# Performance work log

Hardware: AMD Instinct MI355X
Metric: run time of the kernel (lower is better)

## Reference

```python
import jax, jax.numpy as jnp
import numpy as np

N_SENT, B, S, D = 256, 512, 128, 1024
L, LATENT = 10331, 101  # int(sqrt(10331)) == 101


def setup_inputs() -> dict:
    key = jax.random.key(0)
    ks = jax.random.split(key, 16)
    inv = 1.0 / np.sqrt(D)
    return {
        'elmo_outputs': jax.random.normal(ks[0], (N_SENT, S, D), jnp.float32),
        'men_mask': jax.random.randint(ks[1], (B, S), 0, 2).astype(jnp.float32),
        'ctx_mask': jax.random.randint(ks[2], (B, S), 0, 2).astype(jnp.float32),
        'dist': jax.random.uniform(ks[3], (B, S), jnp.float32),
        'gathers': jax.random.randint(ks[4], (B,), 0, N_SENT),
        # nn.Linear weights, stored [out, in] as in torch
        'W_men_m': jax.random.normal(ks[5], (D, D), jnp.float32) * inv,
        'W_men_o': jax.random.normal(ks[6], (1, D), jnp.float32) * inv,
        'W_ctx_c': jax.random.normal(ks[7], (D, D), jnp.float32) * inv,
        'W_ctx_m': jax.random.normal(ks[8], (D, D), jnp.float32) * inv,
        'w_ctx_d': jax.random.normal(ks[9], (D,), jnp.float32),  # Linear(1, D) weight [D,1] squeezed
        'W_ctx_o': jax.random.normal(ks[10], (1, D), jnp.float32) * inv,
        'W_out': jax.random.normal(ks[11], (L, 2 * D), jnp.float32) * (1.0 / np.sqrt(2 * D)),
        'W_f2l': jax.random.normal(ks[12], (LATENT, 2 * D), jnp.float32) * (1.0 / np.sqrt(2 * D)),
        'W_l2l': jax.random.normal(ks[13], (L, LATENT), jnp.float32) * (1.0 / np.sqrt(LATENT)),
        'latent_scalar': jnp.array(0.1, jnp.float32),
    }


def reference(elmo_outputs, men_mask, ctx_mask, dist, gathers,
              W_men_m, W_men_o, W_ctx_c, W_ctx_m, w_ctx_d, W_ctx_o,
              W_out, W_f2l, W_l2l, latent_scalar):
    NEG = -10000.0
    # gather: sentence reps -> mention rows, [B, S, D]
    x = elmo_outputs[gathers]
    # mention additive attention
    men_h = jnp.tanh(jnp.einsum('bsd,ed->bse', x, W_men_m))
    men_score = jnp.einsum('bse,oe->bso', men_h, W_men_o)  # [B,S,1]
    men_score = men_score + (1.0 - men_mask[:, :, None]) * NEG
    men_attn = jax.nn.softmax(men_score, axis=1)
    men_repr = jnp.sum(x * men_attn, axis=1)  # [B, D]
    # context additive attention (dropout layers are identity in eval)
    ctx_h = jnp.tanh(
        jnp.einsum('bsd,ed->bse', x, W_ctx_c)
        + jnp.einsum('bd,ed->be', men_repr, W_ctx_m)[:, None, :]
        + dist[:, :, None] * w_ctx_d
    )
    ctx_score = jnp.einsum('bse,oe->bso', ctx_h, W_ctx_o)
    ctx_score = ctx_score + (1.0 - ctx_mask[:, :, None]) * NEG
    ctx_attn = jax.nn.softmax(ctx_score, axis=1)
    ctx_repr = jnp.sum(x * ctx_attn, axis=1)  # [B, D]
    final_repr = jnp.concatenate([men_repr, ctx_repr], axis=1)  # [B, 2D]
    outputs = final_repr @ W_out.T  # [B, L]
    latent_label = final_repr @ W_f2l.T  # [B, latent]
    outputs_latent = latent_label @ W_l2l.T  # [B, L]
    outputs = outputs + latent_scalar * outputs_latent
    return outputs, outputs_latent
```

## Files before the change

### kernel.cpp

```cpp
#include <hip/hip_runtime.h>
#include <hip/hip_bf16.h>

typedef __bf16 bf16x8 __attribute__((ext_vector_type(8)));
typedef float f32x4 __attribute__((ext_vector_type(4)));
typedef unsigned short u16x8 __attribute__((ext_vector_type(8)));

#define DEV __device__ __forceinline__

static constexpr int N_SENTC = 256, BB = 512, SS = 128, DD = 1024;
static constexpr int LL = 10331, LATENT = 101;
static constexpr int LPAD = 10368;
static constexpr int LATPAD = 128;

DEV float bf2f(unsigned short u) {
  unsigned v = (unsigned)u << 16;
  return __builtin_bit_cast(float, v);
}
DEV unsigned short f2bf(float f) {
  unsigned u = __builtin_bit_cast(unsigned, f);
  unsigned lsb = (u >> 16) & 1u;
  u += 0x7fffu + lsb;
  return (unsigned short)(u >> 16);
}

DEV void stage8(unsigned short* dst, const float* src) {
  float4 a = *(const float4*)src;
  float4 b = *(const float4*)(src + 4);
  unsigned short t[8];
  t[0] = f2bf(a.x); t[1] = f2bf(a.y); t[2] = f2bf(a.z); t[3] = f2bf(a.w);
  t[4] = f2bf(b.x); t[5] = f2bf(b.y); t[6] = f2bf(b.z); t[7] = f2bf(b.w);
  *(uint4*)dst = *(uint4*)t;
}

DEV void gl_lds16(const unsigned short* g, unsigned short* l) {
  __builtin_amdgcn_global_load_lds(
      (const __attribute__((address_space(1))) unsigned int*)g,
      (__attribute__((address_space(3))) unsigned int*)l, 16, 0, 0);
}

__global__ __launch_bounds__(256) void k_cvt(
    const float* __restrict__ src, unsigned short* __restrict__ dst, int n4) {
  for (int i = blockIdx.x * 256 + threadIdx.x; i < n4; i += gridDim.x * 256) {
    float4 v = ((const float4*)src)[i];
    unsigned short t[4] = {f2bf(v.x), f2bf(v.y), f2bf(v.z), f2bf(v.w)};
    ((uint2*)dst)[i] = *(const uint2*)t;
  }
}

__global__ __launch_bounds__(256) void k_cvt_pad(
    const float* __restrict__ src, unsigned short* __restrict__ dst,
    int srcR, int srcC, int dstC, int total) {
  for (int i = blockIdx.x * 256 + threadIdx.x; i < total; i += gridDim.x * 256) {
    int r = i / dstC, c = i - r * dstC;
    dst[i] = (r < srcR && c < srcC) ? f2bf(src[(size_t)r * srcC + c]) : (unsigned short)0;
  }
}

__global__ __launch_bounds__(256) void k_mc_gemm(
    const unsigned short* __restrict__ Xb, const unsigned short* __restrict__ Wmb,
    const unsigned short* __restrict__ Wcb, const float* __restrict__ wo,
    float* __restrict__ score, unsigned short* __restrict__ Hc) {
  __shared__ __align__(16) unsigned short As[2 * 128 * 32];
  __shared__ __align__(16) unsigned short Bs[2 * 128 * 32];
  const int colTile = blockIdx.x;
  const int rowBase = blockIdx.y * 128;
  const bool isMen = colTile < 8;
  const unsigned short* __restrict__ Bsrc = isMen ? Wmb : Wcb;
  const int bcolBase = (isMen ? colTile : colTile - 8) * 128;
  const int tid = threadIdx.x, wave = tid >> 6, lane = tid & 63;
  const int lm = lane & 15, lq = lane >> 4;
  const int wr = (wave & 1) * 64, wc = (wave >> 1) * 64;
  const int srow = wave * 32 + (lane >> 2);
  const int scol = (lane & 3) * 8;
  const unsigned short* aPtr = Xb + (size_t)(rowBase + srow) * 1024 + scol;
  const unsigned short* bPtr = Bsrc + (size_t)(bcolBase + srow) * 1024 + scol;
  f32x4 acc[4][4] = {};
  for (int k0 = 0; k0 < 1024; k0 += 64) {
    __syncthreads();
#pragma unroll
    for (int h = 0; h < 2; ++h) {
      gl_lds16(aPtr + k0 + h * 32, As + h * 4096 + wave * 1024);
      gl_lds16(aPtr + k0 + h * 32 + 16 * 1024, As + h * 4096 + wave * 1024 + 512);
      gl_lds16(bPtr + k0 + h * 32, Bs + h * 4096 + wave * 1024);
      gl_lds16(bPtr + k0 + h * 32 + 16 * 1024, Bs + h * 4096 + wave * 1024 + 512);
    }
    __syncthreads();
#pragma unroll
    for (int h = 0; h < 2; ++h) {
      bf16x8 af[4], bfr[4];
#pragma unroll
      for (int m = 0; m < 4; ++m)
        af[m] = *(const bf16x8*)&As[h * 4096 + (wr + m * 16 + lm) * 32 + lq * 8];
#pragma unroll
      for (int n = 0; n < 4; ++n)
        bfr[n] = *(const bf16x8*)&Bs[h * 4096 + (wc + n * 16 + lm) * 32 + lq * 8];
#pragma unroll
      for (int m = 0; m < 4; ++m)
#pragma unroll
        for (int n = 0; n < 4; ++n)
          acc[m][n] = __builtin_amdgcn_mfma_f32_16x16x32_bf16(af[m], bfr[n], acc[m][n], 0, 0, 0);
    }
  }
  if (isMen) {
    float wov[4];
#pragma unroll
    for (int n = 0; n < 4; ++n) wov[n] = wo[bcolBase + wc + n * 16 + lm];
    float rsum[4][4];
#pragma unroll
    for (int m = 0; m < 4; ++m)
#pragma unroll
      for (int r = 0; r < 4; ++r) {
        float s = 0.f;
#pragma unroll
        for (int n = 0; n < 4; ++n) s += tanhf(acc[m][n][r]) * wov[n];
        rsum[m][r] = s;
      }
#pragma unroll
    for (int msk = 1; msk <= 8; msk <<= 1)
#pragma unroll
      for (int m = 0; m < 4; ++m)
#pragma unroll
        for (int r = 0; r < 4; ++r) rsum[m][r] += __shfl_xor(rsum[m][r], msk, 64);
    if (lm == 0) {
#pragma unroll
      for (int m = 0; m < 4; ++m)
#pragma unroll
        for (int r = 0; r < 4; ++r)
          atomicAdd(&score[rowBase + wr + m * 16 + lq * 4 + r], rsum[m][r]);
    }
  } else {
#pragma unroll
    for (int m = 0; m < 4; ++m)
#pragma unroll
      for (int n = 0; n < 4; ++n) {
        int col = bcolBase + wc + n * 16 + lm;
#pragma unroll
        for (int r = 0; r < 4; ++r) {
          int row = rowBase + wr + m * 16 + lq * 4 + r;
          Hc[(size_t)row * 1024 + col] = f2bf(acc[m][n][r]);
        }
      }
  }
}

__global__ __launch_bounds__(256) void k_ctx_score(
    const unsigned short* __restrict__ Hc, const int* __restrict__ gathers,
    const float* __restrict__ cb, const float* __restrict__ wd,
    const float* __restrict__ wo, const float* __restrict__ dist,
    float* __restrict__ score) {
  const int b = blockIdx.x, tid = threadIdx.x, wave = tid >> 6, lane = tid & 63;
  const int n = gathers[b];
  __shared__ float cbl[1024], wdl[1024], wol[1024];
  for (int i = tid; i < 1024; i += 256) {
    cbl[i] = cb[b * 1024 + i];
    wdl[i] = wd[i];
    wol[i] = wo[i];
  }
  __syncthreads();
  for (int s = wave; s < 128; s += 4) {
    float d = dist[b * 128 + s];
    const unsigned short* hrow = &Hc[(size_t)(n * 128 + s) * 1024 + lane * 16];
    unsigned short hs[16];
    *(uint4*)hs = *(const uint4*)hrow;
    *(uint4*)(hs + 8) = *(const uint4*)(hrow + 8);
    float p = 0.f;
#pragma unroll
    for (int j = 0; j < 16; ++j) {
      int e = lane * 16 + j;
      p += tanhf(bf2f(hs[j]) + cbl[e] + d * wdl[e]) * wol[e];
    }
#pragma unroll
    for (int msk = 1; msk <= 32; msk <<= 1) p += __shfl_xor(p, msk, 64);
    if (lane == 0) score[b * 128 + s] = p;
  }
}

__global__ __launch_bounds__(256) void k_softb(
    const float* __restrict__ score_src, const float* __restrict__ mask,
    const unsigned short* __restrict__ Xb, const int* __restrict__ gathers,
    unsigned short* __restrict__ finalrb, int isCtx) {
  const int b = blockIdx.x, tid = threadIdx.x;
  const int n = gathers[b];
  __shared__ float attn[128];
  __shared__ float red[128 * 8];
  __shared__ float smax, ssum;
  if (tid < 128) {
    int srow = isCtx ? b : n;
    attn[tid] = score_src[srow * 128 + tid] + (1.0f - mask[b * 128 + tid]) * (-10000.0f);
  }
  __syncthreads();
  if (tid == 0) {
    float m = attn[0];
    for (int i = 1; i < 128; ++i) m = fmaxf(m, attn[i]);
    smax = m;
  }
  __syncthreads();
  if (tid < 128) attn[tid] = expf(attn[tid] - smax);
  __syncthreads();
  if (tid == 0) {
    float s = 0.f;
    for (int i = 0; i < 128; ++i) s += attn[i];
    ssum = 1.0f / s;
  }
  __syncthreads();
  if (tid < 128) attn[tid] *= ssum;
  __syncthreads();
  const unsigned short* xb = Xb + (size_t)n * 128 * 1024;
  const int c = tid & 127, h = tid >> 7;
  float acc[8] = {};
  for (int s = h; s < 128; s += 2) {
    float w = attn[s];
    u16x8 v = *(const u16x8*)&xb[(size_t)s * 1024 + c * 8];
#pragma unroll
    for (int j = 0; j < 8; ++j) acc[j] += w * bf2f(v[j]);
  }
  if (h == 1) {
#pragma unroll
    for (int j = 0; j < 8; ++j) red[c * 8 + j] = acc[j];
  }
  __syncthreads();
  if (h == 0) {
    unsigned short o[8];
#pragma unroll
    for (int j = 0; j < 8; ++j) o[j] = f2bf(acc[j] + red[c * 8 + j]);
    *(uint4*)&finalrb[(size_t)b * 2048 + (isCtx ? 1024 : 0) + c * 8] = *(uint4*)o;
  }
}

__global__ __launch_bounds__(256) void k_cb_gemm_b(
    const unsigned short* __restrict__ finalrb, const unsigned short* __restrict__ Wcmb,
    float* __restrict__ cb) {
  __shared__ __align__(16) unsigned short As[64 * 32];
  __shared__ __align__(16) unsigned short Bs[64 * 32];
  const int bid = blockIdx.x;
  const int rowBase = (bid >> 4) * 64, colBase = (bid & 15) * 64;
  const int tid = threadIdx.x, wave = tid >> 6, lane = tid & 63;
  const int lm = lane & 15, lq = lane >> 4;
  const int sr = tid >> 2, sc = (tid & 3) * 8;
  f32x4 acc[4] = {};
  for (int k0 = 0; k0 < 1024; k0 += 32) {
    __syncthreads();
    *(uint4*)&As[sr * 32 + sc] = *(const uint4*)&finalrb[(size_t)(rowBase + sr) * 2048 + k0 + sc];
    *(uint4*)&Bs[sr * 32 + sc] = *(const uint4*)&Wcmb[(size_t)(colBase + sr) * 1024 + k0 + sc];
    __syncthreads();
    bf16x8 af = *(const bf16x8*)&As[(wave * 16 + lm) * 32 + lq * 8];
#pragma unroll
    for (int j = 0; j < 4; ++j) {
      bf16x8 bfr = *(const bf16x8*)&Bs[(j * 16 + lm) * 32 + lq * 8];
      acc[j] = __builtin_amdgcn_mfma_f32_16x16x32_bf16(af, bfr, acc[j], 0, 0, 0);
    }
  }
#pragma unroll
  for (int j = 0; j < 4; ++j) {
    int col = colBase + j * 16 + lm;
#pragma unroll
    for (int r = 0; r < 4; ++r) {
      int row = rowBase + wave * 16 + lq * 4 + r;
      cb[row * 1024 + col] = acc[j][r];
    }
  }
}

__global__ __launch_bounds__(256) void k_lat_gemm_b(
    const unsigned short* __restrict__ finalrb, const unsigned short* __restrict__ Wf2lb,
    unsigned short* __restrict__ latb) {
  __shared__ __align__(16) unsigned short As[64 * 32];
  __shared__ __align__(16) unsigned short Bs[64 * 32];
  const int rowBase = blockIdx.y * 64, colBase = blockIdx.x * 64;
  const int tid = threadIdx.x, wave = tid >> 6, lane = tid & 63;
  const int lm = lane & 15, lq = lane >> 4;
  const int sr = tid >> 2, sc = (tid & 3) * 8;
  f32x4 acc[4] = {};
  for (int k0 = 0; k0 < 2048; k0 += 32) {
    __syncthreads();
    *(uint4*)&As[sr * 32 + sc] = *(const uint4*)&finalrb[(size_t)(rowBase + sr) * 2048 + k0 + sc];
    *(uint4*)&Bs[sr * 32 + sc] = *(const uint4*)&Wf2lb[(size_t)(colBase + sr) * 2048 + k0 + sc];
    __syncthreads();
    bf16x8 af = *(const bf16x8*)&As[(wave * 16 + lm) * 32 + lq * 8];
#pragma unroll
    for (int j = 0; j < 4; ++j) {
      bf16x8 bfr = *(const bf16x8*)&Bs[(j * 16 + lm) * 32 + lq * 8];
      acc[j] = __builtin_amdgcn_mfma_f32_16x16x32_bf16(af, bfr, acc[j], 0, 0, 0);
    }
  }
#pragma unroll
  for (int j = 0; j < 4; ++j) {
    int col = colBase + j * 16 + lm;
#pragma unroll
    for (int r = 0; r < 4; ++r) {
      int row = rowBase + wave * 16 + lq * 4 + r;
      latb[row * LATPAD + col] = f2bf(acc[j][r]);
    }
  }
}

__global__ __launch_bounds__(256) void k_out_gemm_b(
    const unsigned short* __restrict__ finalrb, const unsigned short* __restrict__ Woutb,
    const unsigned short* __restrict__ latb, const unsigned short* __restrict__ Wl2lb,
    const float* __restrict__ lscale, float* __restrict__ out,
    float* __restrict__ outLat) {
  __shared__ __align__(16) unsigned short As[2 * 128 * 32];
  __shared__ __align__(16) unsigned short Bs[2 * 128 * 32];
  const int colBase = blockIdx.x * 128;
  const int rowBase = blockIdx.y * 128;
  const int tid = threadIdx.x, wave = tid >> 6, lane = tid & 63;
  const int lm = lane & 15, lq = lane >> 4;
  const int wr = (wave & 1) * 64, wc = (wave >> 1) * 64;
  const int srow = wave * 32 + (lane >> 2);
  const int scol = (lane & 3) * 8;
  const float scal = lscale[0];
  const unsigned short* aPtr = finalrb + (size_t)(rowBase + srow) * 2048 + scol;
  const unsigned short* bPtr = Woutb + (size_t)(colBase + srow) * 2048 + scol;
  f32x4 acc[4][4] = {};
  for (int k0 = 0; k0 < 2048; k0 += 64) {
    __syncthreads();
#pragma unroll
    for (int h = 0; h < 2; ++h) {
      gl_lds16(aPtr + k0 + h * 32, As + h * 4096 + wave * 1024);
      gl_lds16(aPtr + k0 + h * 32 + 16 * 2048, As + h * 4096 + wave * 1024 + 512);
      gl_lds16(bPtr + k0 + h * 32, Bs + h * 4096 + wave * 1024);
      gl_lds16(bPtr + k0 + h * 32 + 16 * 2048, Bs + h * 4096 + wave * 1024 + 512);
    }
    __syncthreads();
#pragma unroll
    for (int h = 0; h < 2; ++h) {
      bf16x8 af[4], bfr[4];
#pragma unroll
      for (int m = 0; m < 4; ++m)
        af[m] = *(const bf16x8*)&As[h * 4096 + (wr + m * 16 + lm) * 32 + lq * 8];
#pragma unroll
      for (int n = 0; n < 4; ++n)
        bfr[n] = *(const bf16x8*)&Bs[h * 4096 + (wc + n * 16 + lm) * 32 + lq * 8];
#pragma unroll
      for (int m = 0; m < 4; ++m)
#pragma unroll
        for (int n = 0; n < 4; ++n)
          acc[m][n] = __builtin_amdgcn_mfma_f32_16x16x32_bf16(af[m], bfr[n], acc[m][n], 0, 0, 0);
    }
  }
  const unsigned short* aPtr2 = latb + (size_t)(rowBase + srow) * LATPAD + scol;
  const unsigned short* bPtr2 = Wl2lb + (size_t)(colBase + srow) * LATPAD + scol;
  f32x4 acc2[4][4] = {};
  for (int k0 = 0; k0 < 128; k0 += 64) {
    __syncthreads();
#pragma unroll
    for (int h = 0; h < 2; ++h) {
      gl_lds16(aPtr2 + k0 + h * 32, As + h * 4096 + wave * 1024);
      gl_lds16(aPtr2 + k0 + h * 32 + 16 * LATPAD, As + h * 4096 + wave * 1024 + 512);
      gl_lds16(bPtr2 + k0 + h * 32, Bs + h * 4096 + wave * 1024);
      gl_lds16(bPtr2 + k0 + h * 32 + 16 * LATPAD, Bs + h * 4096 + wave * 1024 + 512);
    }
    __syncthreads();
#pragma unroll
    for (int h = 0; h < 2; ++h) {
      bf16x8 af[4], bfr[4];
#pragma unroll
      for (int m = 0; m < 4; ++m)
        af[m] = *(const bf16x8*)&As[h * 4096 + (wr + m * 16 + lm) * 32 + lq * 8];
#pragma unroll
      for (int n = 0; n < 4; ++n)
        bfr[n] = *(const bf16x8*)&Bs[h * 4096 + (wc + n * 16 + lm) * 32 + lq * 8];
#pragma unroll
      for (int m = 0; m < 4; ++m)
#pragma unroll
        for (int n = 0; n < 4; ++n)
          acc2[m][n] = __builtin_amdgcn_mfma_f32_16x16x32_bf16(af[m], bfr[n], acc2[m][n], 0, 0, 0);
    }
  }
#pragma unroll
  for (int m = 0; m < 4; ++m)
#pragma unroll
    for (int n = 0; n < 4; ++n) {
      int col = colBase + wc + n * 16 + lm;
      if (col < LL) {
#pragma unroll
        for (int r = 0; r < 4; ++r) {
          int row = rowBase + wr + m * 16 + lq * 4 + r;
          float lv = acc2[m][n][r];
          out[(size_t)row * LL + col] = acc[m][n][r] + scal * lv;
          outLat[(size_t)row * LL + col] = lv;
        }
      }
    }
}

__global__ __launch_bounds__(256) void k_men_gemm(
    const float* __restrict__ X, const float* __restrict__ Wm,
    const float* __restrict__ wo, float* __restrict__ score) {
  __shared__ __align__(16) unsigned short As[64 * 32];
  __shared__ __align__(16) unsigned short Bs[64 * 32];
  const int bid = blockIdx.x;
  const int rowBase = (bid >> 4) * 64, colBase = (bid & 15) * 64;
  const int tid = threadIdx.x, wave = tid >> 6, lane = tid & 63;
  const int lm = lane & 15, lq = lane >> 4;
  const int sr = tid >> 2, sc = (tid & 3) * 8;
  f32x4 acc[4] = {};
  for (int k0 = 0; k0 < 1024; k0 += 32) {
    __syncthreads();
    stage8(&As[sr * 32 + sc], &X[(size_t)(rowBase + sr) * 1024 + k0 + sc]);
    stage8(&Bs[sr * 32 + sc], &Wm[(size_t)(colBase + sr) * 1024 + k0 + sc]);
    __syncthreads();
    bf16x8 af = *(const bf16x8*)&As[(wave * 16 + lm) * 32 + lq * 8];
#pragma unroll
    for (int j = 0; j < 4; ++j) {
      bf16x8 bfr = *(const bf16x8*)&Bs[(j * 16 + lm) * 32 + lq * 8];
      acc[j] = __builtin_amdgcn_mfma_f32_16x16x32_bf16(af, bfr, acc[j], 0, 0, 0);
    }
  }
  float rsum[4] = {0.f, 0.f, 0.f, 0.f};
#pragma unroll
  for (int j = 0; j < 4; ++j) {
    float w = wo[colBase + j * 16 + lm];
#pragma unroll
    for (int r = 0; r < 4; ++r) rsum[r] += tanhf(acc[j][r]) * w;
  }
#pragma unroll
  for (int m = 1; m <= 8; m <<= 1)
#pragma unroll
    for (int r = 0; r < 4; ++r) rsum[r] += __shfl_xor(rsum[r], m, 64);
  if (lm == 0) {
    int row0 = rowBase + wave * 16 + lq * 4;
#pragma unroll
    for (int r = 0; r < 4; ++r) atomicAdd(&score[row0 + r], rsum[r]);
  }
}

__global__ __launch_bounds__(256) void k_ctx_gemm(
    const float* __restrict__ X, const int* __restrict__ gathers,
    const float* __restrict__ Wc, const float* __restrict__ wd,
    const float* __restrict__ wo, const float* __restrict__ dist,
    const float* __restrict__ cb, float* __restrict__ score) {
  __shared__ __align__(16) unsigned short As[64 * 32];
  __shared__ __align__(16) unsigned short Bs[64 * 32];
  const int bid = blockIdx.x;
  const int rowBase = (bid >> 4) * 64, colBase = (bid & 15) * 64;
  const int tid = threadIdx.x, wave = tid >> 6, lane = tid & 63;
  const int lm = lane & 15, lq = lane >> 4;
  const int sr = tid >> 2, sc = (tid & 3) * 8;
  const int row_g = rowBase + sr;
  const int srcRow = (gathers[row_g >> 7] << 7) + (row_g & 127);
  f32x4 acc[4] = {};
  for (int k0 = 0; k0 < 1024; k0 += 32) {
    __syncthreads();
    stage8(&As[sr * 32 + sc], &X[(size_t)srcRow * 1024 + k0 + sc]);
    stage8(&Bs[sr * 32 + sc], &Wc[(size_t)(colBase + sr) * 1024 + k0 + sc]);
    __syncthreads();
    bf16x8 af = *(const bf16x8*)&As[(wave * 16 + lm) * 32 + lq * 8];
#pragma unroll
    for (int j = 0; j < 4; ++j) {
      bf16x8 bfr = *(const bf16x8*)&Bs[(j * 16 + lm) * 32 + lq * 8];
      acc[j] = __builtin_amdgcn_mfma_f32_16x16x32_bf16(af, bfr, acc[j], 0, 0, 0);
    }
  }
  float rsum[4] = {0.f, 0.f, 0.f, 0.f};
#pragma unroll
  for (int j = 0; j < 4; ++j) {
    int col = colBase + j * 16 + lm;
    float w = wo[col];
    float wdv = wd[col];
#pragma unroll
    for (int r = 0; r < 4; ++r) {
      int rg = rowBase + wave * 16 + lq * 4 + r;
      int b = rg >> 7, s = rg & 127;
      float v = acc[j][r] + cb[b * 1024 + col] + dist[b * 128 + s] * wdv;
      rsum[r] += tanhf(v) * w;
    }
  }
#pragma unroll
  for (int m = 1; m <= 8; m <<= 1)
#pragma unroll
    for (int r = 0; r < 4; ++r) rsum[r] += __shfl_xor(rsum[r], m, 64);
  if (lm == 0) {
    int row0 = rowBase + wave * 16 + lq * 4;
#pragma unroll
    for (int r = 0; r < 4; ++r) atomicAdd(&score[row0 + r], rsum[r]);
  }
}

__global__ __launch_bounds__(256) void k_soft(
    const float* __restrict__ score_src, const float* __restrict__ mask,
    const float* __restrict__ X, const int* __restrict__ gathers,
    float* __restrict__ finalr, int isCtx) {
  const int b = blockIdx.x, tid = threadIdx.x;
  const int n = gathers[b];
  __shared__ float attn[128];
  __shared__ float smax, ssum;
  if (tid < 128) {
    int srow = isCtx ? b : n;
    attn[tid] = score_src[srow * 128 + tid] + (1.0f - mask[b * 128 + tid]) * (-10000.0f);
  }
  __syncthreads();
  if (tid == 0) {
    float m = attn[0];
    for (int i = 1; i < 128; ++i) m = fmaxf(m, attn[i]);
    smax = m;
  }
  __syncthreads();
  if (tid < 128) attn[tid] = expf(attn[tid] - smax);
  __syncthreads();
  if (tid == 0) {
    float s = 0.f;
    for (int i = 0; i < 128; ++i) s += attn[i];
    ssum = 1.0f / s;
  }
  __syncthreads();
  if (tid < 128) attn[tid] *= ssum;
  __syncthreads();
  const float* xb = &X[(size_t)(n << 7) * 1024];
  const int off = isCtx ? 1024 : 0;
  for (int d = tid; d < 1024; d += 256) {
    float a = 0.f;
#pragma unroll 8
    for (int s = 0; s < 128; ++s) a += attn[s] * xb[s * 1024 + d];
    finalr[b * 2048 + off + d] = a;
  }
}

__global__ __launch_bounds__(256) void k_cb_gemm(
    const float* __restrict__ finalr, const float* __restrict__ Wcm,
    float* __restrict__ cb) {
  __shared__ __align__(16) unsigned short As[64 * 32];
  __shared__ __align__(16) unsigned short Bs[64 * 32];
  const int bid = blockIdx.x;
  const int rowBase = (bid >> 4) * 64, colBase = (bid & 15) * 64;
  const int tid = threadIdx.x, wave = tid >> 6, lane = tid & 63;
  const int lm = lane & 15, lq = lane >> 4;
  const int sr = tid >> 2, sc = (tid & 3) * 8;
  f32x4 acc[4] = {};
  for (int k0 = 0; k0 < 1024; k0 += 32) {
    __syncthreads();
    stage8(&As[sr * 32 + sc], &finalr[(size_t)(rowBase + sr) * 2048 + k0 + sc]);
    stage8(&Bs[sr * 32 + sc], &Wcm[(size_t)(colBase + sr) * 1024 + k0 + sc]);
    __syncthreads();
    bf16x8 af = *(const bf16x8*)&As[(wave * 16 + lm) * 32 + lq * 8];
#pragma unroll
    for (int j = 0; j < 4; ++j) {
      bf16x8 bfr = *(const bf16x8*)&Bs[(j * 16 + lm) * 32 + lq * 8];
      acc[j] = __builtin_amdgcn_mfma_f32_16x16x32_bf16(af, bfr, acc[j], 0, 0, 0);
    }
  }
#pragma unroll
  for (int j = 0; j < 4; ++j) {
    int col = colBase + j * 16 + lm;
#pragma unroll
    for (int r = 0; r < 4; ++r) {
      int row = rowBase + wave * 16 + lq * 4 + r;
      cb[row * 1024 + col] = acc[j][r];
    }
  }
}

__global__ __launch_bounds__(256) void k_lat_gemm(
    const float* __restrict__ finalr, const float* __restrict__ Wf2l,
    float* __restrict__ lat) {
  __shared__ __align__(16) unsigned short As[64 * 32];
  __shared__ __align__(16) unsigned short Bs[64 * 32];
  const int rowBase = blockIdx.y * 64, colBase = blockIdx.x * 64;
  const int tid = threadIdx.x, wave = tid >> 6, lane = tid & 63;
  const int lm = lane & 15, lq = lane >> 4;
  const int sr = tid >> 2, sc = (tid & 3) * 8;
  f32x4 acc[4] = {};
  for (int k0 = 0; k0 < 2048; k0 += 32) {
    __syncthreads();
    stage8(&As[sr * 32 + sc], &finalr[(size_t)(rowBase + sr) * 2048 + k0 + sc]);
    int l = colBase + sr;
    if (l < LATENT) {
      stage8(&Bs[sr * 32 + sc], &Wf2l[(size_t)l * 2048 + k0 + sc]);
    } else {
      uint4 z = {0, 0, 0, 0};
      *(uint4*)&Bs[sr * 32 + sc] = z;
    }
    __syncthreads();
    bf16x8 af = *(const bf16x8*)&As[(wave * 16 + lm) * 32 + lq * 8];
#pragma unroll
    for (int j = 0; j < 4; ++j) {
      bf16x8 bfr = *(const bf16x8*)&Bs[(j * 16 + lm) * 32 + lq * 8];
      acc[j] = __builtin_amdgcn_mfma_f32_16x16x32_bf16(af, bfr, acc[j], 0, 0, 0);
    }
  }
#pragma unroll
  for (int j = 0; j < 4; ++j) {
    int col = colBase + j * 16 + lm;
    if (col < LATENT) {
#pragma unroll
      for (int r = 0; r < 4; ++r) {
        int row = rowBase + wave * 16 + lq * 4 + r;
        lat[row * LATENT + col] = acc[j][r];
      }
    }
  }
}

__global__ __launch_bounds__(256) void k_out_gemm(
    const float* __restrict__ finalr, const float* __restrict__ Wout,
    const float* __restrict__ lat, const float* __restrict__ Wl2l,
    const float* __restrict__ lscale, float* __restrict__ out,
    float* __restrict__ outLat) {
  __shared__ __align__(16) unsigned short As[64 * 32];
  __shared__ __align__(16) unsigned short Bs[64 * 32];
  const int rowBase = blockIdx.y * 64, colBase = blockIdx.x * 64;
  const int tid = threadIdx.x, wave = tid >> 6, lane = tid & 63;
  const int lm = lane & 15, lq = lane >> 4;
  const int sr = tid >> 2, sc = (tid & 3) * 8;
  const float scal = lscale[0];
  const int lrow = colBase + sr;
  const bool lvalid = (lrow < LL);
  f32x4 acc[4] = {};
  for (int k0 = 0; k0 < 2048; k0 += 32) {
    __syncthreads();
    stage8(&As[sr * 32 + sc], &finalr[(size_t)(rowBase + sr) * 2048 + k0 + sc]);
    if (lvalid) {
      stage8(&Bs[sr * 32 + sc], &Wout[(size_t)lrow * 2048 + k0 + sc]);
    } else {
      uint4 z = {0, 0, 0, 0};
      *(uint4*)&Bs[sr * 32 + sc] = z;
    }
    __syncthreads();
    bf16x8 af = *(const bf16x8*)&As[(wave * 16 + lm) * 32 + lq * 8];
#pragma unroll
    for (int j = 0; j < 4; ++j) {
      bf16x8 bfr = *(const bf16x8*)&Bs[(j * 16 + lm) * 32 + lq * 8];
      acc[j] = __builtin_amdgcn_mfma_f32_16x16x32_bf16(af, bfr, acc[j], 0, 0, 0);
    }
  }
  f32x4 acc2[4] = {};
  for (int k2 = 0; k2 < 128; k2 += 32) {
    __syncthreads();
    const int brow = rowBase + sr;
#pragma unroll
    for (int jj = 0; jj < 8; ++jj) {
      int idx = k2 + sc + jj;
      As[sr * 32 + sc + jj] = (idx < LATENT) ? f2bf(lat[brow * LATENT + idx]) : (unsigned short)0;
      Bs[sr * 32 + sc + jj] = (lvalid && idx < LATENT) ? f2bf(Wl2l[lrow * LATENT + idx]) : (unsigned short)0;
    }
    __syncthreads();
    bf16x8 af = *(const bf16x8*)&As[(wave * 16 + lm) * 32 + lq * 8];
#pragma unroll
    for (int j = 0; j < 4; ++j) {
      bf16x8 bfr = *(const bf16x8*)&Bs[(j * 16 + lm) * 32 + lq * 8];
      acc2[j] = __builtin_amdgcn_mfma_f32_16x16x32_bf16(af, bfr, acc2[j], 0, 0, 0);
    }
  }
#pragma unroll
  for (int j = 0; j < 4; ++j) {
    int col = colBase + j * 16 + lm;
    if (col < LL) {
#pragma unroll
      for (int r = 0; r < 4; ++r) {
        int row = rowBase + wave * 16 + lq * 4 + r;
        float lv = acc2[j][r];
        out[(size_t)row * LL + col] = acc[j][r] + scal * lv;
        outLat[(size_t)row * LL + col] = lv;
      }
    }
  }
}

extern "C" void kernel_launch(void* const* d_in, const int* in_sizes, int n_in,
                              void* d_out, int out_size, void* d_ws, size_t ws_size,
                              hipStream_t stream) {
  const float* X = (const float*)d_in[0];
  const float* men_mask = (const float*)d_in[1];
  const float* ctx_mask = (const float*)d_in[2];
  const float* dist = (const float*)d_in[3];
  const int* gathers = (const int*)d_in[4];
  const float* W_men_m = (const float*)d_in[5];
  const float* W_men_o = (const float*)d_in[6];
  const float* W_ctx_c = (const float*)d_in[7];
  const float* W_ctx_m = (const float*)d_in[8];
  const float* w_ctx_d = (const float*)d_in[9];
  const float* W_ctx_o = (const float*)d_in[10];
  const float* W_out = (const float*)d_in[11];
  const float* W_f2l = (const float*)d_in[12];
  const float* W_l2l = (const float*)d_in[13];
  const float* lscale = (const float*)d_in[14];
  float* out = (float*)d_out;
  float* outLat = out + (size_t)BB * LL;

  size_t off = 0;
  auto carve = [&](size_t bytes) {
    void* p = (char*)d_ws + off;
    off = (off + bytes + 255) & ~(size_t)255;
    return p;
  };
  float* sent_score = (float*)carve(32768 * 4);
  float* ctx_score = (float*)carve(65536 * 4);
  float* finalr = (float*)carve((size_t)512 * 2048 * 4);
  float* cb = (float*)carve((size_t)512 * 1024 * 4);
  float* lat = (float*)carve((size_t)512 * LATENT * 4);
  unsigned short* Xb = (unsigned short*)carve((size_t)32768 * 1024 * 2);
  unsigned short* Wmb = (unsigned short*)carve((size_t)1024 * 1024 * 2);
  unsigned short* Wcb = (unsigned short*)carve((size_t)1024 * 1024 * 2);
  unsigned short* Wcmb = (unsigned short*)carve((size_t)1024 * 1024 * 2);
  unsigned short* Hc = (unsigned short*)carve((size_t)32768 * 1024 * 2);
  unsigned short* Wf2lb = (unsigned short*)carve((size_t)LATPAD * 2048 * 2);
  unsigned short* Wl2lb = (unsigned short*)carve((size_t)LPAD * LATPAD * 2);
  unsigned short* finalrb = (unsigned short*)carve((size_t)512 * 2048 * 2);
  unsigned short* latb = (unsigned short*)carve((size_t)512 * LATPAD * 2);
  const bool fits = off <= ws_size;
  unsigned short* Woutb = Xb;

  if (fits) {
    hipMemsetAsync(sent_score, 0, 32768 * sizeof(float), stream);
    k_cvt<<<8192, 256, 0, stream>>>(X, Xb, 32768 * 1024 / 4);
    k_cvt<<<1024, 256, 0, stream>>>(W_men_m, Wmb, 1024 * 1024 / 4);
    k_cvt<<<1024, 256, 0, stream>>>(W_ctx_c, Wcb, 1024 * 1024 / 4);
    k_cvt<<<1024, 256, 0, stream>>>(W_ctx_m, Wcmb, 1024 * 1024 / 4);
    k_cvt_pad<<<512, 256, 0, stream>>>(W_f2l, Wf2lb, LATENT, 2048, 2048, LATPAD * 2048);
    k_cvt_pad<<<1024, 256, 0, stream>>>(W_l2l, Wl2lb, LL, LATENT, LATPAD, LPAD * LATPAD);
    k_mc_gemm<<<dim3(16, 256), 256, 0, stream>>>(Xb, Wmb, Wcb, W_men_o, sent_score, Hc);
    k_softb<<<512, 256, 0, stream>>>(sent_score, men_mask, Xb, gathers, finalrb, 0);
    k_cb_gemm_b<<<128, 256, 0, stream>>>(finalrb, Wcmb, cb);
    k_ctx_score<<<512, 256, 0, stream>>>(Hc, gathers, cb, w_ctx_d, W_ctx_o, dist, ctx_score);
    k_softb<<<512, 256, 0, stream>>>(ctx_score, ctx_mask, Xb, gathers, finalrb, 1);
    k_lat_gemm_b<<<dim3(2, 8), 256, 0, stream>>>(finalrb, Wf2lb, latb);
    k_cvt_pad<<<8192, 256, 0, stream>>>(W_out, Woutb, LL, 2048, 2048, LPAD * 2048);
    k_out_gemm_b<<<dim3(81, 4), 256, 0, stream>>>(finalrb, Woutb, latb, Wl2lb,
                                                  lscale, out, outLat);
  } else {
    hipMemsetAsync(d_ws, 0, (32768 + 65536) * sizeof(float), stream);
    k_men_gemm<<<8192, 256, 0, stream>>>(X, W_men_m, W_men_o, sent_score);
    k_soft<<<512, 256, 0, stream>>>(sent_score, men_mask, X, gathers, finalr, 0);
    k_cb_gemm<<<128, 256, 0, stream>>>(finalr, W_ctx_m, cb);
    k_ctx_gemm<<<16384, 256, 0, stream>>>(X, gathers, W_ctx_c, w_ctx_d, W_ctx_o, dist, cb, ctx_score);
    k_soft<<<512, 256, 0, stream>>>(ctx_score, ctx_mask, X, gathers, finalr, 1);
    k_lat_gemm<<<dim3(2, 8), 256, 0, stream>>>(finalr, W_f2l, lat);
    k_out_gemm<<<dim3(162, 8), 256, 0, stream>>>(finalr, W_out, lat, W_l2l, lscale, out, outLat);
  }
}
```

Before: 740.9 us.

## Rewrite mention/context GEMM as 256x256 8-wave pipelined kernel with swizzled LDS

Replaces the 128x128 tile, 4-wave GEMM with a 256x256 tile, 8-wave kernel. It double-buffers LDS, interleaves global-to-LDS loads with MFMA phases, and uses s_setprio and manual vmcnt waits. LDS columns are XOR-swizzled to avoid bank conflicts, and block IDs are remapped so blocks sharing weight tiles run close together for L2 reuse. The goal is better MFMA utilisation and less memory stall on the largest GEMM, at the cost of more registers and fragile hand-written barrier and wait counts.

```diff
diff --git a/kernel.cpp b/kernel.cpp
--- a/kernel.cpp
+++ b/kernel.cpp
@@ -56,58 +56,131 @@
   }
 }
 
-__global__ __launch_bounds__(256) void k_mc_gemm(
+__global__ __launch_bounds__(512) void k_mc_gemm8(
     const unsigned short* __restrict__ Xb, const unsigned short* __restrict__ Wmb,
     const unsigned short* __restrict__ Wcb, const float* __restrict__ wo,
     float* __restrict__ score, unsigned short* __restrict__ Hc) {
-  __shared__ __align__(16) unsigned short As[2 * 128 * 32];
-  __shared__ __align__(16) unsigned short Bs[2 * 128 * 32];
-  const int colTile = blockIdx.x;
-  const int rowBase = blockIdx.y * 128;
-  const bool isMen = colTile < 8;
+  __shared__ __align__(16) unsigned short lds[2][2][2][8192];
+  const int bid = blockIdx.x;
+  const int lbid = (bid & 7) * 128 + (bid >> 3);
+  const int colTile = lbid & 7, rowTile = lbid >> 3;
+  const int rowBase = rowTile * 256;
+  const bool isMen = colTile < 4;
   const unsigned short* __restrict__ Bsrc = isMen ? Wmb : Wcb;
-  const int bcolBase = (isMen ? colTile : colTile - 8) * 128;
-  const int tid = threadIdx.x, wave = tid >> 6, lane = tid & 63;
+  const int bcolBase = (colTile & 3) * 256;
+  const int tid = threadIdx.x, w = tid >> 6, lane = tid & 63;
   const int lm = lane & 15, lq = lane >> 4;
-  const int wr = (wave & 1) * 64, wc = (wave >> 1) * 64;
-  const int srow = wave * 32 + (lane >> 2);
-  const int scol = (lane & 3) * 8;
-  const unsigned short* aPtr = Xb + (size_t)(rowBase + srow) * 1024 + scol;
-  const unsigned short* bPtr = Bsrc + (size_t)(bcolBase + srow) * 1024 + scol;
-  f32x4 acc[4][4] = {};
-  for (int k0 = 0; k0 < 1024; k0 += 64) {
-    __syncthreads();
-#pragma unroll
-    for (int h = 0; h < 2; ++h) {
-      gl_lds16(aPtr + k0 + h * 32, As + h * 4096 + wave * 1024);
-      gl_lds16(aPtr + k0 + h * 32 + 16 * 1024, As + h * 4096 + wave * 1024 + 512);
-      gl_lds16(bPtr + k0 + h * 32, Bs + h * 4096 + wave * 1024);
-      gl_lds16(bPtr + k0 + h * 32 + 16 * 1024, Bs + h * 4096 + wave * 1024 + 512);
-    }
-    __syncthreads();
-#pragma unroll
-    for (int h = 0; h < 2; ++h) {
-      bf16x8 af[4], bfr[4];
-#pragma unroll
-      for (int m = 0; m < 4; ++m)
-        af[m] = *(const bf16x8*)&As[h * 4096 + (wr + m * 16 + lm) * 32 + lq * 8];
-#pragma unroll
-      for (int n = 0; n < 4; ++n)
-        bfr[n] = *(const bf16x8*)&Bs[h * 4096 + (wc + n * 16 + lm) * 32 + lq * 8];
-#pragma unroll
-      for (int m = 0; m < 4; ++m)
-#pragma unroll
-        for (int n = 0; n < 4; ++n)
-          acc[m][n] = __builtin_amdgcn_mfma_f32_16x16x32_bf16(af[m], bfr[n], acc[m][n], 0, 0, 0);
-    }
-  }
+  const int wr = w >> 2, wc = w & 3;
+  const int stRow = w * 16 + (lane >> 2);
+  const int stCol = ((lane & 3) * 8) ^ ((lane >> 5) << 4);
+  const unsigned short* aSrc = Xb + (size_t)(rowBase + stRow) * 1024 + stCol;
+  const unsigned short* bSrc = Bsrc + (size_t)(bcolBase + stRow) * 1024 + stCol;
+  const int rdCol = (lq * 16) ^ ((lane & 8) ? 32 : 0);
+  const int aoff = (wr * 16 + lm) * 64 + rdCol;
+  const int boff = (wc * 16 + lm) * 64 + rdCol;
+  f32x4 acc[8][4] = {};
+
+  auto ST = [&](int op, int h, int kt, int buf) {
+    const unsigned short* s = (op ? bSrc : aSrc) + (size_t)h * 131072 + kt * 64;
+    unsigned short* d = &lds[buf][op][h][w * 512];
+    gl_lds16(s, d);
+    gl_lds16(s + 32, d + 4096);
+  };
+
+  ST(0, 0, 0, 0); ST(1, 0, 0, 0); ST(0, 1, 0, 0); ST(1, 1, 0, 0);
+  ST(0, 0, 1, 1); ST(1, 0, 1, 1); ST(0, 1, 1, 1);
+  asm volatile("s_waitcnt vmcnt(6)" ::: "memory");
+  __builtin_amdgcn_s_barrier();
+
+  bf16x8 af[4][2], bfr[4][2];
+  for (int kt = 0; kt < 16; ++kt) {
+    const int buf = kt & 1;
+    const char* A0 = (const char*)&lds[buf][0][0][0];
+    const char* A1 = (const char*)&lds[buf][0][1][0];
+    const char* B0 = (const char*)&lds[buf][1][0][0];
+    const char* B1 = (const char*)&lds[buf][1][1][0];
+#pragma unroll
+    for (int m = 0; m < 4; ++m)
+#pragma unroll
+      for (int ks = 0; ks < 2; ++ks)
+        af[m][ks] = *(const bf16x8*)(A0 + aoff + m * 2048 + ks * 8192);
+#pragma unroll
+    for (int n = 0; n < 2; ++n)
+#pragma unroll
+      for (int ks = 0; ks < 2; ++ks)
+        bfr[n][ks] = *(const bf16x8*)(B0 + boff + n * 4096 + ks * 8192);
+    if (kt + 1 < 16) ST(1, 1, kt + 1, buf ^ 1);
+    __builtin_amdgcn_s_barrier();
+    __builtin_amdgcn_s_setprio(1);
+#pragma unroll
+    for (int m = 0; m < 4; ++m)
+#pragma unroll
+      for (int n = 0; n < 2; ++n)
+#pragma unroll
+        for (int ks = 0; ks < 2; ++ks)
+          acc[m][n] = __builtin_amdgcn_mfma_f32_16x16x32_bf16(af[m][ks], bfr[n][ks], acc[m][n], 0, 0, 0);
+    __builtin_amdgcn_s_setprio(0);
+    __builtin_amdgcn_s_barrier();
+#pragma unroll
+    for (int n = 0; n < 2; ++n)
+#pragma unroll
+      for (int ks = 0; ks < 2; ++ks)
+        bfr[2 + n][ks] = *(const bf16x8*)(B1 + boff + n * 4096 + ks * 8192);
+    if (kt + 2 < 16) ST(0, 0, kt + 2, buf);
+    __builtin_amdgcn_s_barrier();
+    __builtin_amdgcn_s_setprio(1);
+#pragma unroll
+    for (int m = 0; m < 4; ++m)
+#pragma unroll
+      for (int n = 0; n < 2; ++n)
+#pragma unroll
+        for (int ks = 0; ks < 2; ++ks)
+          acc[m][2 + n] = __builtin_amdgcn_mfma_f32_16x16x32_bf16(af[m][ks], bfr[2 + n][ks], acc[m][2 + n], 0, 0, 0);
+    __builtin_amdgcn_s_setprio(0);
+    __builtin_amdgcn_s_barrier();
+#pragma unroll
+    for (int m = 0; m < 4; ++m)
+#pragma unroll
+      for (int ks = 0; ks < 2; ++ks)
+        af[m][ks] = *(const bf16x8*)(A1 + aoff + m * 2048 + ks * 8192);
+    if (kt + 2 < 16) ST(1, 0, kt + 2, buf);
+    __builtin_amdgcn_s_barrier();
+    __builtin_amdgcn_s_setprio(1);
+#pragma unroll
+    for (int m = 0; m < 4; ++m)
+#pragma unroll
+      for (int n = 0; n < 2; ++n)
+#pragma unroll
+        for (int ks = 0; ks < 2; ++ks)
+          acc[4 + m][n] = __builtin_amdgcn_mfma_f32_16x16x32_bf16(af[m][ks], bfr[n][ks], acc[4 + m][n], 0, 0, 0);
+    __builtin_amdgcn_s_setprio(0);
+    __builtin_amdgcn_s_barrier();
+    if (kt + 2 < 16) ST(0, 1, kt + 2, buf);
+    __builtin_amdgcn_s_barrier();
+    __builtin_amdgcn_s_setprio(1);
+#pragma unroll
+    for (int m = 0; m < 4; ++m)
+#pragma unroll
+      for (int n = 0; n < 2; ++n)
+#pragma unroll
+        for (int ks = 0; ks < 2; ++ks)
+          acc[4 + m][2 + n] = __builtin_amdgcn_mfma_f32_16x16x32_bf16(af[m][ks], bfr[2 + n][ks], acc[4 + m][2 + n], 0, 0, 0);
+    __builtin_amdgcn_s_setprio(0);
+    if (kt < 14) {
+      asm volatile("s_waitcnt vmcnt(6)" ::: "memory");
+    } else {
+      asm volatile("s_waitcnt vmcnt(0)" ::: "memory");
+    }
+    __builtin_amdgcn_s_barrier();
+  }
+
   if (isMen) {
     float wov[4];
 #pragma unroll
-    for (int n = 0; n < 4; ++n) wov[n] = wo[bcolBase + wc + n * 16 + lm];
-    float rsum[4][4];
-#pragma unroll
-    for (int m = 0; m < 4; ++m)
+    for (int n = 0; n < 4; ++n) wov[n] = wo[bcolBase + n * 64 + wc * 16 + lm];
+    float rsum[8][4];
+#pragma unroll
+    for (int m = 0; m < 8; ++m)
 #pragma unroll
       for (int r = 0; r < 4; ++r) {
         float s = 0.f;
@@ -118,28 +191,29 @@
 #pragma unroll
     for (int msk = 1; msk <= 8; msk <<= 1)
 #pragma unroll
-      for (int m = 0; m < 4; ++m)
+      for (int m = 0; m < 8; ++m)
 #pragma unroll
         for (int r = 0; r < 4; ++r) rsum[m][r] += __shfl_xor(rsum[m][r], msk, 64);
     if (lm == 0) {
 #pragma unroll
-      for (int m = 0; m < 4; ++m)
+      for (int m = 0; m < 8; ++m)
 #pragma unroll
         for (int r = 0; r < 4; ++r)
-          atomicAdd(&score[rowBase + wr + m * 16 + lq * 4 + r], rsum[m][r]);
+          atomicAdd(&score[rowBase + m * 32 + wr * 16 + lq * 4 + r], rsum[m][r]);
     }
   } else {
-#pragma unroll
-    for (int m = 0; m < 4; ++m)
+    const int cb0 = (colTile - 4) * 256 + wc * 16 + lm;
+#pragma unroll
+    for (int m = 0; m < 8; ++m) {
+      const int row = rowBase + m * 32 + wr * 16 + lq * 4;
 #pragma unroll
       for (int n = 0; n < 4; ++n) {
-        int col = bcolBase + wc + n * 16 + lm;
-#pragma unroll
-        for (int r = 0; r < 4; ++r) {
-          int row = rowBase + wr + m * 16 + lq * 4 + r;
-          Hc[(size_t)row * 1024 + col] = f2bf(acc[m][n][r]);
-        }
+        const int col = cb0 + n * 64;
+#pragma unroll
+        for (int r = 0; r < 4; ++r)
+          Hc[(size_t)(row + r) * 1024 + col] = f2bf(acc[m][n][r]);
       }
+    }
   }
 }
 
@@ -708,7 +782,7 @@
     k_cvt<<<1024, 256, 0, stream>>>(W_ctx_m, Wcmb, 1024 * 1024 / 4);
     k_cvt_pad<<<512, 256, 0, stream>>>(W_f2l, Wf2lb, LATENT, 2048, 2048, LATPAD * 2048);
     k_cvt_pad<<<1024, 256, 0, stream>>>(W_l2l, Wl2lb, LL, LATENT, LATPAD, LPAD * LATPAD);
-    k_mc_gemm<<<dim3(16, 256), 256, 0, stream>>>(Xb, Wmb, Wcb, W_men_o, sent_score, Hc);
+    k_mc_gemm8<<<1024, 512, 0, stream>>>(Xb, Wmb, Wcb, W_men_o, sent_score, Hc);
     k_softb<<<512, 256, 0, stream>>>(sent_score, men_mask, Xb, gathers, finalrb, 0);
     k_cb_gemm_b<<<128, 256, 0, stream>>>(finalrb, Wcmb, cb);
     k_ctx_score<<<512, 256, 0, stream>>>(Hc, gathers, cb, w_ctx_d, W_ctx_o, dist, ctx_score);
```

Measured after the change: 708.9 us. -4.3%, faster.
